# Performance work log

Measured on AMD Instinct MI355X. Metric: run time of the kernel, lower is better.

## Reference

```python
import jax, jax.numpy as jnp
import numpy as np

B, T, D, H = 8, 1024, 1024, 16

def setup_inputs() -> dict:
    key = jax.random.key(0)
    k1, k2, k3, k4, k5 = jax.random.split(key, 5)
    x = jax.random.normal(k1, (B, T, D), dtype=jnp.float32)
    mask = jnp.tril(jnp.ones((T, T), dtype=bool))[None, None]  # [1,1,T,T] causal
    s = 0.02
    W_attn = jax.random.normal(k2, (D, 3 * D), dtype=jnp.float32) * s
    b_attn = jnp.zeros((3 * D,), dtype=jnp.float32)
    W_proj = jax.random.normal(k3, (D, D), dtype=jnp.float32) * s
    b_proj = jnp.zeros((D,), dtype=jnp.float32)
    return {"x": x, "mask": mask, "W_attn": W_attn, "b_attn": b_attn,
            "W_proj": W_proj, "b_proj": b_proj}

def reference(x, mask, W_attn, b_attn, W_proj, b_proj):
    num_heads = H
    b, t, d = x.shape
    hd = d // num_heads
    qkv = x @ W_attn + b_attn                      # [b,t,3d]
    q, k, v = jnp.split(qkv, 3, axis=-1)
    def to_heads(a):
        return a.reshape(b, t, num_heads, hd).transpose(0, 2, 1, 3)  # [b,h,t,hd]
    q, k, v = to_heads(q), to_heads(k), to_heads(v)
    scale = 1.0 / jnp.sqrt(jnp.float32(hd))
    attn = jnp.einsum('bhqd,bhkd->bhqk', q, k) * scale
    attn = jnp.where(mask, attn, jnp.finfo(jnp.float32).min)
    attn = jax.nn.softmax(attn, axis=-1)
    o = jnp.einsum('bhqk,bhkd->bhqd', attn, v)
    o = o.transpose(0, 2, 1, 3).reshape(b, t, d)   # [b,t,d]
    return o @ W_proj + b_proj
```

## Files before the change

### kernel.cpp

```cpp
#include <hip/hip_runtime.h>
#include <cstdint>


typedef __attribute__((ext_vector_type(8))) short bf16x8;
typedef __attribute__((ext_vector_type(4))) float f32x4;

__device__ __forceinline__ short f2b(float x) {
  unsigned u = __builtin_bit_cast(unsigned, x);
  u += 0x7fffu + ((u >> 16) & 1u);
  return (short)(u >> 16);
}

__device__ __forceinline__ void gl2lds16(short* l, const short* g) {
  __builtin_amdgcn_global_load_lds(
      (const __attribute__((address_space(1))) void*)g,
      (__attribute__((address_space(3))) void*)l, 16, 0, 0);
}


__global__ void f32_to_bf16_vec(const float* __restrict__ in,
                                short* __restrict__ outb, int n4) {
  int i = blockIdx.x * 256 + threadIdx.x;
  if (i >= n4) return;
  float4 v = ((const float4*)in)[i];
  short4 o;
  o.x = f2b(v.x); o.y = f2b(v.y); o.z = f2b(v.z); o.w = f2b(v.w);
  ((short4*)outb)[i] = o;
}

__global__ void transpose_f32_bf16(const float* __restrict__ in,
                                   short* __restrict__ out, int R, int C) {
  __shared__ float tile[32][33];
  int c0 = blockIdx.x * 32, r0 = blockIdx.y * 32;
  int tx = threadIdx.x, ty = threadIdx.y;
#pragma unroll
  for (int i = 0; i < 32; i += 8)
    tile[ty + i][tx] = in[(long)(r0 + ty + i) * C + c0 + tx];
  __syncthreads();
#pragma unroll
  for (int i = 0; i < 32; i += 8)
    out[(long)(c0 + ty + i) * R + r0 + tx] = f2b(tile[tx][ty + i]);
}


template <int EPI>
__global__ __launch_bounds__(256, 3) void gemm_bt(
    const short* __restrict__ A, const short* __restrict__ Bt,
    const float* __restrict__ bias, float* __restrict__ outF,
    short* __restrict__ qh, short* __restrict__ kh, short* __restrict__ vT,
    int M, int N, int K) {
  __shared__ short At[128 * 64];
  __shared__ short Bl[128 * 64];
  const int t = threadIdx.x;
  const int wave = t >> 6, lane = t & 63;
  const int quad = lane >> 4, l15 = lane & 15;
  const int wr = wave >> 1, wc = wave & 1;
  const int m0 = blockIdx.y * 128, n0 = blockIdx.x * 128;

  f32x4 acc[4][4] = {};

  const int srow = t >> 3;
  const int sch0 = t & 7;

  for (int k0 = 0; k0 < K; k0 += 64) {
    __syncthreads();
#pragma unroll
    for (int c = 0; c < 4; ++c) {
      int row = c * 32 + srow;
      int ch = sch0 ^ (row & 7);
      gl2lds16(At + (c * 256 + t) * 8, A + (long)(m0 + row) * K + k0 + ch * 8);
      gl2lds16(Bl + (c * 256 + t) * 8, Bt + (long)(n0 + row) * K + k0 + ch * 8);
    }
    asm volatile("s_waitcnt vmcnt(0)" ::: "memory");
    __syncthreads();

#pragma unroll
    for (int s = 0; s < 2; ++s) {
      const int cx = (s * 4 + quad) ^ (l15 & 7);
      bf16x8 af[4], bfr[4];
#pragma unroll
      for (int i = 0; i < 4; ++i)
        af[i] = *(const bf16x8*)(At + (wr * 64 + i * 16 + l15) * 64 + cx * 8);
#pragma unroll
      for (int j = 0; j < 4; ++j)
        bfr[j] = *(const bf16x8*)(Bl + (wc * 64 + j * 16 + l15) * 64 + cx * 8);
#pragma unroll
      for (int i = 0; i < 4; ++i)
#pragma unroll
        for (int j = 0; j < 4; ++j)
          acc[i][j] = __builtin_amdgcn_mfma_f32_16x16x32_bf16(af[i], bfr[j],
                                                              acc[i][j], 0, 0, 0);
    }
  }

  if (EPI == 1) {
#pragma unroll
    for (int j = 0; j < 4; ++j) {
      int col = n0 + wc * 64 + j * 16 + l15;
      float bv = bias[col];
#pragma unroll
      for (int i = 0; i < 4; ++i)
#pragma unroll
        for (int r = 0; r < 4; ++r) {
          int row = m0 + wr * 64 + i * 16 + quad * 4 + r;
          outF[(long)row * N + col] = acc[i][j][r] + bv;
        }
    }
  } else {
    const int sec = n0 >> 10;
    const int b = m0 >> 10;
#pragma unroll
    for (int j = 0; j < 4; ++j) {
      int col = n0 + wc * 64 + j * 16 + l15;
      float bv = bias[col];
      int d = col & 1023, h = d >> 6, dh = d & 63;
      if (sec == 2) {
        long base = ((long)(b * 16 + h) * 64 + dh) * 1024;
#pragma unroll
        for (int i = 0; i < 4; ++i) {
          int tt0 = (m0 & 1023) + wr * 64 + i * 16 + quad * 4;
          short4 v;
          v.x = f2b(acc[i][j][0] + bv);
          v.y = f2b(acc[i][j][1] + bv);
          v.z = f2b(acc[i][j][2] + bv);
          v.w = f2b(acc[i][j][3] + bv);
          *(short4*)(vT + base + tt0) = v;
        }
      } else {
        short* dst = (sec == 0) ? qh : kh;
        long hbase = ((long)(b * 16 + h) * 1024) * 64 + dh;
#pragma unroll
        for (int i = 0; i < 4; ++i)
#pragma unroll
          for (int r = 0; r < 4; ++r) {
            int tt = (m0 & 1023) + wr * 64 + i * 16 + quad * 4 + r;
            dst[hbase + (long)tt * 64] = f2b(acc[i][j][r] + bv);
          }
      }
    }
  }
}


__global__ __launch_bounds__(256, 2) void attn_kernel(
    const short* __restrict__ qh, const short* __restrict__ kh,
    const short* __restrict__ vT, short* __restrict__ attout) {
  __shared__ short Kb[2][64 * 64];
  __shared__ short Vb[2][64 * 64];
  __shared__ short P_lds[4][16][64];
  const int p = blockIdx.x;
  const int bh = blockIdx.y;
  const int t = threadIdx.x;
  const int wave = t >> 6, lane = t & 63, quad = lane >> 4, l15 = lane & 15;
  const short* q_head = qh + (long)bh * 1024 * 64;
  const short* k_head = kh + (long)bh * 1024 * 64;
  const short* v_head = vT + (long)bh * 64 * 1024;
  const int b_ = bh >> 4, h_ = bh & 15;
  const float sl = 0.125f * 1.44269504089f;

  const int qt[4] = {p, 7 - p, 8 + p, 15 - p};

  auto stage = [&](int kt, int buf) {
    const int kk0 = kt * 64;
#pragma unroll
    for (int i = 0; i < 2; ++i) {
      int s = i * 256 + t;
      int row = s >> 3, cg = (s & 7) ^ (row & 7);
      gl2lds16(&Kb[buf][s * 8], k_head + (kk0 + row) * 64 + cg * 8);
    }
#pragma unroll
    for (int i = 0; i < 2; ++i) {
      int s = i * 256 + t;
      int row = s >> 3, cg = (s & 7) ^ (row & 7);
      gl2lds16(&Vb[buf][s * 8], v_head + row * 1024 + kk0 + cg * 8);
    }
  };

  bf16x8 qf[4][2];
#pragma unroll
  for (int i = 0; i < 4; ++i) {
    int qb = qt[i] * 64 + wave * 16;
#pragma unroll
    for (int s = 0; s < 2; ++s)
      qf[i][s] = *(const bf16x8*)(q_head + (qb + l15) * 64 + s * 32 + quad * 8);
  }

  float l[4] = {};
  f32x4 o[4][4] = {};

  stage(0, 0);
  __syncthreads();

  const int nkt = qt[3] + 1;

#pragma unroll 1
  for (int kt = 0; kt < nkt; ++kt) {
    const int buf = kt & 1;
    const short* Kt = Kb[buf];
    const short* Vt = Vb[buf];

    bf16x8 kfr[4][2];
#pragma unroll
    for (int jj = 0; jj < 4; ++jj) {
      int row = jj * 16 + l15;
#pragma unroll
      for (int s = 0; s < 2; ++s) {
        int off = ((s * 4 + quad) ^ (row & 7)) * 8;
        kfr[jj][s] = *(const bf16x8*)(Kt + row * 64 + off);
      }
    }
    bf16x8 vfr[4][2];
    {
      const int qh2 = quad >> 1, ql4 = (quad & 1) * 4;
#pragma unroll
      for (int dj = 0; dj < 4; ++dj) {
        int row = dj * 16 + l15, r7 = row & 7;
        const short* vr = Vt + row * 64;
        short4 a0 = *(const short4*)(vr + ((qh2 ^ r7) * 8) + ql4);
        short4 a1 = *(const short4*)(vr + (((2 + qh2) ^ r7) * 8) + ql4);
        short4 a2 = *(const short4*)(vr + (((4 + qh2) ^ r7) * 8) + ql4);
        short4 a3 = *(const short4*)(vr + (((6 + qh2) ^ r7) * 8) + ql4);
        bf16x8 v0, v1;
        v0[0] = a0.x; v0[1] = a0.y; v0[2] = a0.z; v0[3] = a0.w;
        v0[4] = a1.x; v0[5] = a1.y; v0[6] = a1.z; v0[7] = a1.w;
        v1[0] = a2.x; v1[1] = a2.y; v1[2] = a2.z; v1[3] = a2.w;
        v1[4] = a3.x; v1[5] = a3.y; v1[6] = a3.z; v1[7] = a3.w;
        vfr[dj][0] = v0;
        vfr[dj][1] = v1;
      }
    }

    if (kt + 1 < nkt) stage(kt + 1, buf ^ 1);

#pragma unroll
    for (int i = 0; i < 4; ++i) {
      if (kt <= qt[i]) {
        f32x4 s4[4] = {};
#pragma unroll
        for (int jj = 0; jj < 4; ++jj) {
          s4[jj] = __builtin_amdgcn_mfma_f32_16x16x32_bf16(kfr[jj][0], qf[i][0],
                                                           s4[jj], 0, 0, 0);
          s4[jj] = __builtin_amdgcn_mfma_f32_16x16x32_bf16(kfr[jj][1], qf[i][1],
                                                           s4[jj], 0, 0, 0);
        }
        const bool diag = (kt == qt[i]);
        const int qg = qt[i] * 64 + wave * 16 + l15;
        bf16x8 pf0, pf1;
        float ls = 0.f;
#pragma unroll
        for (int jj = 0; jj < 4; ++jj) {
          const int kbase = kt * 64 + jj * 16 + quad * 4;
#pragma unroll
          for (int r = 0; r < 4; ++r) {
            float sv = s4[jj][r] * sl;
            if (diag && (kbase + r) > qg) sv = -1e30f;
            float e = __builtin_amdgcn_exp2f(sv);
            ls += e;
            short bv = f2b(e);
            if (jj < 2) pf0[(jj & 1) * 4 + r] = bv;
            else pf1[(jj & 1) * 4 + r] = bv;
          }
        }
        l[i] += ls;
#pragma unroll
        for (int dj = 0; dj < 4; ++dj) {
          o[i][dj] = __builtin_amdgcn_mfma_f32_16x16x32_bf16(pf0, vfr[dj][0],
                                                             o[i][dj], 0, 0, 0);
          o[i][dj] = __builtin_amdgcn_mfma_f32_16x16x32_bf16(pf1, vfr[dj][1],
                                                             o[i][dj], 0, 0, 0);
        }
      }
    }
    __syncthreads();
  }

#pragma unroll
  for (int i = 0; i < 4; ++i) {
    l[i] += __shfl_xor(l[i], 16);
    l[i] += __shfl_xor(l[i], 32);
  }

  const int erow = lane >> 3, ech = lane & 7;
#pragma unroll
  for (int i = 0; i < 4; ++i) {
    float inv[4];
#pragma unroll
    for (int r = 0; r < 4; ++r) {
      float lr = __shfl(l[i], quad * 4 + r);
      inv[r] = __builtin_amdgcn_rcpf(lr);
    }
    const int qb = qt[i] * 64 + wave * 16;
#pragma unroll
    for (int dj = 0; dj < 4; ++dj) {
      int ch = dj * 2 + (l15 >> 3), co = l15 & 7;
#pragma unroll
      for (int r = 0; r < 4; ++r) {
        int row = quad * 4 + r;
        P_lds[wave][row][(ch ^ (row & 7)) * 8 + co] = f2b(o[i][dj][r] * inv[r]);
      }
    }
    asm volatile("s_waitcnt lgkmcnt(0)" ::: "memory");
#pragma unroll
    for (int pass = 0; pass < 2; ++pass) {
      int row = pass * 8 + erow;
      bf16x8 v = *(const bf16x8*)(&P_lds[wave][row][(ech ^ (row & 7)) * 8]);
      long g = (long)b_ * 1024 + qb + row;
      *(bf16x8*)(attout + g * 1024 + h_ * 64 + ech * 8) = v;
    }
    asm volatile("s_waitcnt lgkmcnt(0)" ::: "memory");
  }
}


extern "C" void kernel_launch(void* const* d_in, const int* in_sizes, int n_in,
                              void* d_out, int out_size, void* d_ws,
                              size_t ws_size, hipStream_t stream) {
  const float* x = (const float*)d_in[0];
  const float* W_attn = (const float*)d_in[2];
  const float* b_attn = (const float*)d_in[3];
  const float* W_proj = (const float*)d_in[4];
  const float* b_proj = (const float*)d_in[5];
  float* out = (float*)d_out;

  char* ws = (char*)d_ws;
  const size_t MB = 1u << 20;
  short* xb = (short*)(ws);
  short* WaT = (short*)(ws + 16 * MB);
  short* WpT = (short*)(ws + 22 * MB);
  short* qh = (short*)(ws + 24 * MB);
  short* kh = (short*)(ws + 40 * MB);
  short* vT = (short*)(ws + 56 * MB);
  short* attout = xb;

  f32_to_bf16_vec<<<8192, 256, 0, stream>>>(x, xb, 2097152);
  transpose_f32_bf16<<<dim3(3072 / 32, 1024 / 32), dim3(32, 8), 0, stream>>>(
      W_attn, WaT, 1024, 3072);
  transpose_f32_bf16<<<dim3(1024 / 32, 1024 / 32), dim3(32, 8), 0, stream>>>(
      W_proj, WpT, 1024, 1024);
  gemm_bt<0><<<dim3(3072 / 128, 8192 / 128), 256, 0, stream>>>(
      xb, WaT, b_attn, nullptr, qh, kh, vT, 8192, 3072, 1024);
  attn_kernel<<<dim3(4, 128), 256, 0, stream>>>(qh, kh, vT, attout);
  gemm_bt<1><<<dim3(1024 / 128, 8192 / 128), 256, 0, stream>>>(
      attout, WpT, b_proj, out, nullptr, nullptr, nullptr, 8192, 1024, 1024);
}
```

Baseline: 230.1 us.

## Fuse prep kernels, fold softmax scale into Q, permute V layout, pack bf16

Merges the x conversion and both weight transposes into one launch. Folds the softmax scale and log2e factor into the Q epilogue of the QKV GEMM, and permutes the V^T row order so attention can load V fragments with single 16-byte LDS reads instead of four short4 gathers. It also splits the diagonal and non-diagonal masking paths, converts P with packed v_cvt_pk_bf16_f32 instructions, and swaps the attention grid order so blocks of the same head launch adjacently. The aim is to cut launch overhead, ALU work in the inner loop and LDS instructions, at the cost of relying on a matching V permutation between two kernels.

```diff
diff --git a/kernel.cpp b/kernel.cpp
--- a/kernel.cpp
+++ b/kernel.cpp
@@ -11,6 +11,12 @@
   return (short)(u >> 16);
 }
 
+__device__ __forceinline__ unsigned cvtpk(float lo, float hi) {
+  unsigned d;
+  asm("v_cvt_pk_bf16_f32 %0, %1, %2" : "=v"(d) : "v"(lo), "v"(hi));
+  return d;
+}
+
 __device__ __forceinline__ void gl2lds16(short* l, const short* g) {
   __builtin_amdgcn_global_load_lds(
       (const __attribute__((address_space(1))) void*)g,
@@ -18,21 +24,33 @@
 }
 
 
-__global__ void f32_to_bf16_vec(const float* __restrict__ in,
-                                short* __restrict__ outb, int n4) {
-  int i = blockIdx.x * 256 + threadIdx.x;
-  if (i >= n4) return;
-  float4 v = ((const float4*)in)[i];
-  short4 o;
-  o.x = f2b(v.x); o.y = f2b(v.y); o.z = f2b(v.z); o.w = f2b(v.w);
-  ((short4*)outb)[i] = o;
-}
-
-__global__ void transpose_f32_bf16(const float* __restrict__ in,
-                                   short* __restrict__ out, int R, int C) {
+__global__ void prep_fused(const float* __restrict__ x, short* __restrict__ xb,
+                           const float* __restrict__ Wa, short* __restrict__ WaT,
+                           const float* __restrict__ Wp, short* __restrict__ WpT) {
   __shared__ float tile[32][33];
-  int c0 = blockIdx.x * 32, r0 = blockIdx.y * 32;
-  int tx = threadIdx.x, ty = threadIdx.y;
+  const int bid = blockIdx.x;
+  const int t = threadIdx.x;
+  if (bid < 8192) {
+    int i = bid * 256 + t;
+    float4 v = ((const float4*)x)[i];
+    short4 o;
+    o.x = f2b(v.x); o.y = f2b(v.y); o.z = f2b(v.z); o.w = f2b(v.w);
+    ((short4*)xb)[i] = o;
+    return;
+  }
+  const float* in;
+  short* out;
+  int C, bx, by;
+  if (bid < 11264) {
+    int id = bid - 8192;
+    in = Wa; out = WaT; C = 3072; bx = id % 96; by = id / 96;
+  } else {
+    int id = bid - 11264;
+    in = Wp; out = WpT; C = 1024; bx = id % 32; by = id / 32;
+  }
+  const int R = 1024;
+  int c0 = bx * 32, r0 = by * 32;
+  int tx = t & 31, ty = t >> 5;
 #pragma unroll
   for (int i = 0; i < 32; i += 8)
     tile[ty + i][tx] = in[(long)(r0 + ty + i) * C + c0 + tx];
@@ -109,6 +127,7 @@
   } else {
     const int sec = n0 >> 10;
     const int b = m0 >> 10;
+    const float sc = (sec == 0) ? (0.125f * 1.44269504089f) : 1.0f;
 #pragma unroll
     for (int j = 0; j < 4; ++j) {
       int col = n0 + wc * 64 + j * 16 + l15;
@@ -118,7 +137,7 @@
         long base = ((long)(b * 16 + h) * 64 + dh) * 1024;
 #pragma unroll
         for (int i = 0; i < 4; ++i) {
-          int tt0 = (m0 & 1023) + wr * 64 + i * 16 + quad * 4;
+          int tt0 = (m0 & 1023) + wr * 64 + (i >> 1) * 32 + quad * 8 + (i & 1) * 4;
           short4 v;
           v.x = f2b(acc[i][j][0] + bv);
           v.y = f2b(acc[i][j][1] + bv);
@@ -134,7 +153,7 @@
 #pragma unroll
           for (int r = 0; r < 4; ++r) {
             int tt = (m0 & 1023) + wr * 64 + i * 16 + quad * 4 + r;
-            dst[hbase + (long)tt * 64] = f2b(acc[i][j][r] + bv);
+            dst[hbase + (long)tt * 64] = f2b((acc[i][j][r] + bv) * sc);
           }
       }
     }
@@ -148,15 +167,14 @@
   __shared__ short Kb[2][64 * 64];
   __shared__ short Vb[2][64 * 64];
   __shared__ short P_lds[4][16][64];
-  const int p = blockIdx.x;
-  const int bh = blockIdx.y;
+  const int bh = blockIdx.x;
+  const int p = blockIdx.y;
   const int t = threadIdx.x;
   const int wave = t >> 6, lane = t & 63, quad = lane >> 4, l15 = lane & 15;
   const short* q_head = qh + (long)bh * 1024 * 64;
   const short* k_head = kh + (long)bh * 1024 * 64;
   const short* v_head = vT + (long)bh * 64 * 1024;
   const int b_ = bh >> 4, h_ = bh & 15;
-  const float sl = 0.125f * 1.44269504089f;
 
   const int qt[4] = {p, 7 - p, 8 + p, 15 - p};
 
@@ -199,7 +217,7 @@
     const short* Kt = Kb[buf];
     const short* Vt = Vb[buf];
 
-    bf16x8 kfr[4][2];
+    bf16x8 kfr[4][2], vfr[4][2];
 #pragma unroll
     for (int jj = 0; jj < 4; ++jj) {
       int row = jj * 16 + l15;
@@ -207,26 +225,7 @@
       for (int s = 0; s < 2; ++s) {
         int off = ((s * 4 + quad) ^ (row & 7)) * 8;
         kfr[jj][s] = *(const bf16x8*)(Kt + row * 64 + off);
-      }
-    }
-    bf16x8 vfr[4][2];
-    {
-      const int qh2 = quad >> 1, ql4 = (quad & 1) * 4;
-#pragma unroll
-      for (int dj = 0; dj < 4; ++dj) {
-        int row = dj * 16 + l15, r7 = row & 7;
-        const short* vr = Vt + row * 64;
-        short4 a0 = *(const short4*)(vr + ((qh2 ^ r7) * 8) + ql4);
-        short4 a1 = *(const short4*)(vr + (((2 + qh2) ^ r7) * 8) + ql4);
-        short4 a2 = *(const short4*)(vr + (((4 + qh2) ^ r7) * 8) + ql4);
-        short4 a3 = *(const short4*)(vr + (((6 + qh2) ^ r7) * 8) + ql4);
-        bf16x8 v0, v1;
-        v0[0] = a0.x; v0[1] = a0.y; v0[2] = a0.z; v0[3] = a0.w;
-        v0[4] = a1.x; v0[5] = a1.y; v0[6] = a1.z; v0[7] = a1.w;
-        v1[0] = a2.x; v1[1] = a2.y; v1[2] = a2.z; v1[3] = a2.w;
-        v1[4] = a3.x; v1[5] = a3.y; v1[6] = a3.z; v1[7] = a3.w;
-        vfr[dj][0] = v0;
-        vfr[dj][1] = v1;
+        vfr[jj][s] = *(const bf16x8*)(Vt + row * 64 + off);
       }
     }
 
@@ -243,25 +242,43 @@
           s4[jj] = __builtin_amdgcn_mfma_f32_16x16x32_bf16(kfr[jj][1], qf[i][1],
                                                            s4[jj], 0, 0, 0);
         }
-        const bool diag = (kt == qt[i]);
-        const int qg = qt[i] * 64 + wave * 16 + l15;
-        bf16x8 pf0, pf1;
+        float ev[4][4];
         float ls = 0.f;
-#pragma unroll
-        for (int jj = 0; jj < 4; ++jj) {
-          const int kbase = kt * 64 + jj * 16 + quad * 4;
-#pragma unroll
-          for (int r = 0; r < 4; ++r) {
-            float sv = s4[jj][r] * sl;
-            if (diag && (kbase + r) > qg) sv = -1e30f;
-            float e = __builtin_amdgcn_exp2f(sv);
-            ls += e;
-            short bv = f2b(e);
-            if (jj < 2) pf0[(jj & 1) * 4 + r] = bv;
-            else pf1[(jj & 1) * 4 + r] = bv;
+        if (kt == qt[i]) {
+          const int qg = qt[i] * 64 + wave * 16 + l15;
+#pragma unroll
+          for (int jj = 0; jj < 4; ++jj) {
+            const int kb = kt * 64 + jj * 16 + quad * 4;
+#pragma unroll
+            for (int r = 0; r < 4; ++r) {
+              float e = __builtin_amdgcn_exp2f(s4[jj][r]);
+              if (kb + r > qg) e = 0.f;
+              ev[jj][r] = e;
+              ls += e;
+            }
           }
+        } else {
+#pragma unroll
+          for (int jj = 0; jj < 4; ++jj)
+#pragma unroll
+            for (int r = 0; r < 4; ++r) {
+              float e = __builtin_amdgcn_exp2f(s4[jj][r]);
+              ev[jj][r] = e;
+              ls += e;
+            }
         }
         l[i] += ls;
+        int4 pd0, pd1;
+        pd0.x = (int)cvtpk(ev[0][0], ev[0][1]);
+        pd0.y = (int)cvtpk(ev[0][2], ev[0][3]);
+        pd0.z = (int)cvtpk(ev[1][0], ev[1][1]);
+        pd0.w = (int)cvtpk(ev[1][2], ev[1][3]);
+        pd1.x = (int)cvtpk(ev[2][0], ev[2][1]);
+        pd1.y = (int)cvtpk(ev[2][2], ev[2][3]);
+        pd1.z = (int)cvtpk(ev[3][0], ev[3][1]);
+        pd1.w = (int)cvtpk(ev[3][2], ev[3][3]);
+        bf16x8 pf0 = __builtin_bit_cast(bf16x8, pd0);
+        bf16x8 pf1 = __builtin_bit_cast(bf16x8, pd1);
 #pragma unroll
         for (int dj = 0; dj < 4; ++dj) {
           o[i][dj] = __builtin_amdgcn_mfma_f32_16x16x32_bf16(pf0, vfr[dj][0],
@@ -332,14 +349,10 @@
   short* vT = (short*)(ws + 56 * MB);
   short* attout = xb;
 
-  f32_to_bf16_vec<<<8192, 256, 0, stream>>>(x, xb, 2097152);
-  transpose_f32_bf16<<<dim3(3072 / 32, 1024 / 32), dim3(32, 8), 0, stream>>>(
-      W_attn, WaT, 1024, 3072);
-  transpose_f32_bf16<<<dim3(1024 / 32, 1024 / 32), dim3(32, 8), 0, stream>>>(
-      W_proj, WpT, 1024, 1024);
+  prep_fused<<<12288, 256, 0, stream>>>(x, xb, W_attn, WaT, W_proj, WpT);
   gemm_bt<0><<<dim3(3072 / 128, 8192 / 128), 256, 0, stream>>>(
       xb, WaT, b_attn, nullptr, qh, kh, vT, 8192, 3072, 1024);
-  attn_kernel<<<dim3(4, 128), 256, 0, stream>>>(qh, kh, vT, attout);
+  attn_kernel<<<dim3(128, 4), 256, 0, stream>>>(qh, kh, vT, attout);
   gemm_bt<1><<<dim3(1024 / 128, 8192 / 128), 256, 0, stream>>>(
       attout, WpT, b_proj, out, nullptr, nullptr, nullptr, 8192, 1024, 1024);
 }
```

Measured after the change: 201.8 us. 1.14x faster.
